# Optimization experiments

Measured on AMD Instinct MI355X. Metric: run time of the kernel, lower is better.

## Reference

```python
import jax, jax.numpy as jnp
import numpy as np

DIM = 1024
NUM_HEADS = 16
HEAD_DIM = DIM // NUM_HEADS
SCALE = HEAD_DIM ** -0.5


def setup_inputs() -> dict:
    key = jax.random.key(0)
    ks = jax.random.split(key, 9)
    s = 1.0 / np.sqrt(DIM)
    x = jax.random.normal(ks[0], (2, 2048, DIM), dtype=jnp.float32)
    Wq = jax.random.normal(ks[1], (DIM, DIM), dtype=jnp.float32) * s
    Wk = jax.random.normal(ks[2], (DIM, DIM), dtype=jnp.float32) * s
    Wv = jax.random.normal(ks[3], (DIM, DIM), dtype=jnp.float32) * s
    Wp = jax.random.normal(ks[4], (DIM, DIM), dtype=jnp.float32) * s
    bq = jax.random.normal(ks[5], (DIM,), dtype=jnp.float32) * s
    bk = jax.random.normal(ks[6], (DIM,), dtype=jnp.float32) * s
    bv = jax.random.normal(ks[7], (DIM,), dtype=jnp.float32) * s
    bp = jax.random.normal(ks[8], (DIM,), dtype=jnp.float32) * s
    return {"x": x, "Wq": Wq, "bq": bq, "Wk": Wk, "bk": bk,
            "Wv": Wv, "bv": bv, "Wp": Wp, "bp": bp}


def reference(x, Wq, bq, Wk, bk, Wv, bv, Wp, bp):
    B, L, C = x.shape
    H, D = NUM_HEADS, HEAD_DIM
    # Linear projections (torch Linear: x @ W.T + b)
    q = x @ Wq.T + bq
    k = x @ Wk.T + bk
    v = x @ Wv.T + bv
    # (B, L, H*D) -> (B, H, L, D)
    q = q.reshape(B, L, H, D).transpose(0, 2, 1, 3)
    k = k.reshape(B, L, H, D).transpose(0, 2, 1, 3)
    v = v.reshape(B, L, H, D).transpose(0, 2, 1, 3)
    # scaled dot-product attention, full L x L scores (as in source)
    attn = jnp.einsum('bhqd,bhkd->bhqk', q, k) * SCALE
    attn = jax.nn.softmax(attn, axis=-1)
    out = jnp.einsum('bhqk,bhkd->bhqd', attn, v)
    out = out.transpose(0, 2, 1, 3).reshape(B, L, C)
    return out @ Wp.T + bp
```

## Files before the change

### kernel.cpp

```cpp
#include <hip/hip_runtime.h>

#define DIMC 1024
#define SEQL 2048
#define NB   2
#define NH   16
#define HD   64
#define MTOT (NB*SEQL)
#define XSTR 2048
static constexpr float SM_SCALE = 0.125f;
static constexpr float LOG2E    = 1.4426950408889634f;
static constexpr float QSCALE   = SM_SCALE * LOG2E;

typedef short s16x8 __attribute__((ext_vector_type(8)));
typedef short s16x4 __attribute__((ext_vector_type(4)));
typedef float f32x4 __attribute__((ext_vector_type(4)));
typedef int   i32x4 __attribute__((ext_vector_type(4)));

__device__ __forceinline__ unsigned short f2bf(float f) {
    unsigned int u = __float_as_uint(f);
    u += 0x7fffu + ((u >> 16) & 1u);
    return (unsigned short)(u >> 16);
}
__device__ __forceinline__ s16x8 ld8(const unsigned short* p) {
    return *(const s16x8*)p;
}
__device__ __forceinline__ void gld_lds16(const unsigned short* g, unsigned short* l) {
    __builtin_amdgcn_global_load_lds(
        (const __attribute__((address_space(1))) void*)g,
        (__attribute__((address_space(3))) void*)l, 16, 0, 0);
}
__device__ __forceinline__ unsigned int cvtpk(float lo, float hi) {
    unsigned int r;
    asm("v_cvt_pk_bf16_f32 %0, %1, %2" : "=v"(r) : "v"(lo), "v"(hi));
    return r;
}

#define BAR()     asm volatile("s_barrier" ::: "memory")
#define WAITVM8() asm volatile("s_waitcnt vmcnt(8)" ::: "memory")
#define WAITVM4() asm volatile("s_waitcnt vmcnt(4)" ::: "memory")
#define WAITVM0() asm volatile("s_waitcnt vmcnt(0)" ::: "memory")

__global__ __launch_bounds__(256) void cast_all(
    const float* __restrict__ x,
    const float* __restrict__ Wq, const float* __restrict__ Wk,
    const float* __restrict__ Wv, const float* __restrict__ Wp,
    const float* __restrict__ bq, const float* __restrict__ bk,
    const float* __restrict__ bvv,
    unsigned short* __restrict__ xb, unsigned short* __restrict__ wall,
    float* __restrict__ ball)
{
    const int bid = blockIdx.x, tid = threadIdx.x;
    if (bid < 4096) {
        int i = bid * 256 + tid;
        float4 f = ((const float4*)x)[i];
        s16x4 o;
        o[0] = (short)f2bf(f.x); o[1] = (short)f2bf(f.y);
        o[2] = (short)f2bf(f.z); o[3] = (short)f2bf(f.w);
        ((s16x4*)xb)[i] = o;
    } else if (bid < 8192) {
        int j = (bid - 4096) * 256 + tid;
        int r = j >> 18;
        const float* src = (r == 0) ? Wq : (r == 1) ? Wk : (r == 2) ? Wv : Wp;
        float4 f = ((const float4*)src)[j & 262143];
        s16x4 o;
        o[0] = (short)f2bf(f.x); o[1] = (short)f2bf(f.y);
        o[2] = (short)f2bf(f.z); o[3] = (short)f2bf(f.w);
        ((s16x4*)wall)[j] = o;
    } else {
        int t2 = (bid - 8192) * 256 + tid;
        if (t2 < 3072)
            ball[t2] = (t2 < 1024) ? bq[t2]
                     : (t2 < 2048) ? bk[t2 - 1024] : bvv[t2 - 2048];
    }
}

__global__ __launch_bounds__(256) void gemm_tile(
    const unsigned short* __restrict__ A, int astride,
    const unsigned short* __restrict__ Wb,
    const float* __restrict__ bias,
    unsigned short* qk, unsigned short* vtb, float* outf, int mode)
{
    __shared__ __align__(16) unsigned short Asm[3][128 * 32];
    __shared__ __align__(16) unsigned short Bsm[3][128 * 32];

    const int t    = threadIdx.x;
    const int lane = t & 63;
    const int l15  = lane & 15;
    const int quad = lane >> 4;
    const int w    = t >> 6;
    const int mrow = (w & 1) * 64;
    const int ncol = (w >> 1) * 64;
    const int nt_total = (int)gridDim.x >> 5;
    const int xcd = blockIdx.x & 7;
    const int i2  = blockIdx.x >> 3;
    const int nt  = xcd * (nt_total >> 3) + (i2 >> 5);
    const int mt  = i2 & 31;
    const int row0 = mt * 128;

    const unsigned short* ga = A  + (size_t)(row0 + (t >> 2)) * astride + (t & 3) * 8;
    const unsigned short* gb = Wb + (size_t)(nt * 128 + (t >> 2)) * DIMC + (t & 3) * 8;
    const size_t gaStep = (size_t)64 * astride;
    const size_t gbStep = (size_t)64 * DIMC;

    f32x4 acc[4][4] = {};

    auto stage = [&](unsigned short* Ab, unsigned short* Bb, int k0) {
        gld_lds16(ga + k0,          Ab + t * 8);
        gld_lds16(ga + gaStep + k0, Ab + 2048 + t * 8);
        gld_lds16(gb + k0,          Bb + t * 8);
        gld_lds16(gb + gbStep + k0, Bb + 2048 + t * 8);
    };

    auto compute = [&](const unsigned short* Ac, const unsigned short* Bc) {
        s16x8 a[4], b[4];
#pragma unroll
        for (int mi = 0; mi < 4; ++mi)
            a[mi] = *(const s16x8*)(Ac + (mrow + mi * 16 + l15) * 32 + quad * 8);
#pragma unroll
        for (int ni = 0; ni < 4; ++ni)
            b[ni] = *(const s16x8*)(Bc + (ncol + ni * 16 + l15) * 32 + quad * 8);
        __builtin_amdgcn_s_setprio(1);
#pragma unroll
        for (int mi = 0; mi < 4; ++mi)
#pragma unroll
            for (int ni = 0; ni < 4; ++ni)
                acc[mi][ni] = __builtin_amdgcn_mfma_f32_16x16x32_bf16(
                    a[mi], b[ni], acc[mi][ni], 0, 0, 0);
        __builtin_amdgcn_s_setprio(0);
    };

    stage(Asm[0], Bsm[0], 0);
    stage(Asm[1], Bsm[1], 32);

#pragma unroll 1
    for (int k0 = 0; k0 < 960; k0 += 96) {
        stage(Asm[2], Bsm[2], k0 + 64);
        WAITVM8();
        BAR();
        compute(Asm[0], Bsm[0]);
        BAR();
        stage(Asm[0], Bsm[0], k0 + 96);
        WAITVM8();
        BAR();
        compute(Asm[1], Bsm[1]);
        BAR();
        stage(Asm[1], Bsm[1], k0 + 128);
        WAITVM8();
        BAR();
        compute(Asm[2], Bsm[2]);
        BAR();
    }
    WAITVM4();
    BAR();
    compute(Asm[0], Bsm[0]);
    BAR();
    WAITVM0();
    BAR();
    compute(Asm[1], Bsm[1]);

    const int proj = nt >> 3;
#pragma unroll
    for (int ni = 0; ni < 4; ++ni) {
        const int cq = (nt & 7) * 128 + ncol + ni * 16 + l15;
        const float bz = bias[proj * 1024 + cq];
#pragma unroll
        for (int mi = 0; mi < 4; ++mi) {
            const int rbase = row0 + mrow + mi * 16 + quad * 4;
            if (mode == 0) {
                if (proj < 2) {
                    const float scale = (proj == 0) ? QSCALE : 1.0f;
#pragma unroll
                    for (int r = 0; r < 4; ++r)
                        qk[(size_t)(rbase + r) * XSTR + proj * DIMC + cq] =
                            f2bf((acc[mi][ni][r] + bz) * scale);
                } else {
                    const int h = cq >> 6, d = cq & 63;
                    const int bb = rbase >> 11, ll = rbase & (SEQL - 1);
                    s16x4 v4;
                    v4[0] = (short)f2bf(acc[mi][ni][0] + bz);
                    v4[1] = (short)f2bf(acc[mi][ni][1] + bz);
                    v4[2] = (short)f2bf(acc[mi][ni][2] + bz);
                    v4[3] = (short)f2bf(acc[mi][ni][3] + bz);
                    *(s16x4*)(vtb + ((size_t)((bb * NH + h) * HD + d)) * SEQL + ll) = v4;
                }
            } else {
#pragma unroll
                for (int r = 0; r < 4; ++r)
                    outf[(size_t)(rbase + r) * DIMC + cq] = acc[mi][ni][r] + bz;
            }
        }
    }
}

__global__ __launch_bounds__(256) void attn_fused(
    unsigned short* xqk,
    const unsigned short* __restrict__ vt)
{
    __shared__ __align__(16) unsigned short Ksm[2][64 * 64];
    __shared__ __align__(16) unsigned short Vsm[2][64 * 64];

    const int t    = threadIdx.x;
    const int lane = t & 63;
    const int l15  = lane & 15;
    const int quad = lane >> 4;
    const int w    = t >> 6;

    const int xcd = blockIdx.x & 7;
    const int ii  = blockIdx.x >> 3;
    const int bh  = (xcd << 2) | (ii >> 4);
    const int qb  = ii & 15;
    const int h  = bh & (NH - 1);
    const int bb = bh >> 4;
    const int q0A = qb * 128 + w * 16;
    const int q0B = q0A + 64;

    unsigned short* qbase = xqk + (size_t)(bb * SEQL) * XSTR + h * HD + quad * 8;
    unsigned short* qrA = qbase + (size_t)(q0A + l15) * XSTR;
    unsigned short* qrB = qbase + (size_t)(q0B + l15) * XSTR;
    const s16x8 bqA0 = ld8(qrA), bqA1 = ld8(qrA + 32);
    const s16x8 bqB0 = ld8(qrB), bqB1 = ld8(qrB + 32);

    s16x8 bones;
#pragma unroll
    for (int e = 0; e < 8; ++e) bones[e] = (short)0x3F80;

    const int tr = t >> 3, tp = t & 7;
    const int swz = (tp ^ (tr & 7)) * 8;
    const unsigned short* kg = xqk + (size_t)bb * SEQL * XSTR + DIMC + h * HD
                               + (size_t)tr * XSTR + swz;
    const unsigned short* vg = vt + (size_t)(bh * HD + tr) * SEQL + swz;

    f32x4 oA[4] = {}, oB[4] = {};
    f32x4 laccA = {}, laccB = {};
    const int xk = l15 & 7;

    auto stage = [&](unsigned short* Kb, unsigned short* Vb, int j) {
#pragma unroll
        for (int g = 0; g < 2; ++g) {
            gld_lds16(kg + (size_t)(j + g * 32) * XSTR, Kb + g * 2048 + t * 8);
            gld_lds16(vg + (size_t)(g * 32) * SEQL + j,  Vb + g * 2048 + t * 8);
        }
    };

    auto compute = [&](const unsigned short* Kc, const unsigned short* Vc) {
#pragma unroll
        for (int hf = 0; hf < 2; ++hf) {
            const int k0 = (hf * 32 + l15) * 64;
            const int k1 = (hf * 32 + 16 + l15) * 64;
            s16x8 a00 = *(const s16x8*)(Kc + k0 + ((quad       ^ xk) * 8));
            s16x8 a01 = *(const s16x8*)(Kc + k0 + (((quad + 4) ^ xk) * 8));
            s16x8 a10 = *(const s16x8*)(Kc + k1 + ((quad       ^ xk) * 8));
            s16x8 a11 = *(const s16x8*)(Kc + k1 + (((quad + 4) ^ xk) * 8));

            s16x8 bv[4];
#pragma unroll
            for (int c = 0; c < 4; ++c) {
                const unsigned short* va = Vc + (c * 16 + l15) * 64 + (quad & 1) * 4;
                const int kc0 = hf * 4 + (quad >> 1);
                s16x4 v0 = *(const s16x4*)(va + ((kc0       ^ xk) * 8));
                s16x4 v1 = *(const s16x4*)(va + (((kc0 + 2) ^ xk) * 8));
                bv[c] = __builtin_shufflevector(v0, v1, 0, 1, 2, 3, 4, 5, 6, 7);
            }

            __builtin_amdgcn_s_setprio(1);
            {
                f32x4 st0 = {}, st1 = {};
                st0 = __builtin_amdgcn_mfma_f32_16x16x32_bf16(a00, bqA0, st0, 0, 0, 0);
                st0 = __builtin_amdgcn_mfma_f32_16x16x32_bf16(a01, bqA1, st0, 0, 0, 0);
                st1 = __builtin_amdgcn_mfma_f32_16x16x32_bf16(a10, bqA0, st1, 0, 0, 0);
                st1 = __builtin_amdgcn_mfma_f32_16x16x32_bf16(a11, bqA1, st1, 0, 0, 0);
                i32x4 api;
                api[0] = (int)cvtpk(__builtin_amdgcn_exp2f(st0[0]),
                                    __builtin_amdgcn_exp2f(st0[1]));
                api[1] = (int)cvtpk(__builtin_amdgcn_exp2f(st0[2]),
                                    __builtin_amdgcn_exp2f(st0[3]));
                api[2] = (int)cvtpk(__builtin_amdgcn_exp2f(st1[0]),
                                    __builtin_amdgcn_exp2f(st1[1]));
                api[3] = (int)cvtpk(__builtin_amdgcn_exp2f(st1[2]),
                                    __builtin_amdgcn_exp2f(st1[3]));
                s16x8 ap = __builtin_bit_cast(s16x8, api);
                laccA = __builtin_amdgcn_mfma_f32_16x16x32_bf16(ap, bones, laccA, 0, 0, 0);
#pragma unroll
                for (int c = 0; c < 4; ++c)
                    oA[c] = __builtin_amdgcn_mfma_f32_16x16x32_bf16(ap, bv[c], oA[c], 0, 0, 0);
            }
            {
                f32x4 st0 = {}, st1 = {};
                st0 = __builtin_amdgcn_mfma_f32_16x16x32_bf16(a00, bqB0, st0, 0, 0, 0);
                st0 = __builtin_amdgcn_mfma_f32_16x16x32_bf16(a01, bqB1, st0, 0, 0, 0);
                st1 = __builtin_amdgcn_mfma_f32_16x16x32_bf16(a10, bqB0, st1, 0, 0, 0);
                st1 = __builtin_amdgcn_mfma_f32_16x16x32_bf16(a11, bqB1, st1, 0, 0, 0);
                i32x4 api;
                api[0] = (int)cvtpk(__builtin_amdgcn_exp2f(st0[0]),
                                    __builtin_amdgcn_exp2f(st0[1]));
                api[1] = (int)cvtpk(__builtin_amdgcn_exp2f(st0[2]),
                                    __builtin_amdgcn_exp2f(st0[3]));
                api[2] = (int)cvtpk(__builtin_amdgcn_exp2f(st1[0]),
                                    __builtin_amdgcn_exp2f(st1[1]));
                api[3] = (int)cvtpk(__builtin_amdgcn_exp2f(st1[2]),
                                    __builtin_amdgcn_exp2f(st1[3]));
                s16x8 ap = __builtin_bit_cast(s16x8, api);
                laccB = __builtin_amdgcn_mfma_f32_16x16x32_bf16(ap, bones, laccB, 0, 0, 0);
#pragma unroll
                for (int c = 0; c < 4; ++c)
                    oB[c] = __builtin_amdgcn_mfma_f32_16x16x32_bf16(ap, bv[c], oB[c], 0, 0, 0);
            }
            __builtin_amdgcn_s_setprio(0);
        }
    };

    stage(Ksm[0], Vsm[0], 0);

#pragma unroll 1
    for (int jt = 0; jt < SEQL / 64; jt += 2) {
        const int j0 = jt * 64;
        stage(Ksm[1], Vsm[1], j0 + 64);
        WAITVM4();
        BAR();
        compute(Ksm[0], Vsm[0]);
        BAR();
        if (jt + 2 < SEQL / 64) {
            stage(Ksm[0], Vsm[0], j0 + 128);
            WAITVM4();
        } else {
            WAITVM0();
        }
        BAR();
        compute(Ksm[1], Vsm[1]);
        BAR();
    }

    float liA[4], liB[4];
#pragma unroll
    for (int r = 0; r < 4; ++r) {
        liA[r] = 1.0f / laccA[r];
        liB[r] = 1.0f / laccB[r];
    }

#pragma unroll
    for (int c = 0; c < 4; ++c) {
        const int d = c * 16 + l15;
#pragma unroll
        for (int r = 0; r < 4; ++r) {
            const int qr = quad * 4 + r;
            xqk[(size_t)(bb * SEQL + q0A + qr) * XSTR + h * HD + d] = f2bf(oA[c][r] * liA[r]);
            xqk[(size_t)(bb * SEQL + q0B + qr) * XSTR + h * HD + d] = f2bf(oB[c][r] * liB[r]);
        }
    }
}

extern "C" void kernel_launch(void* const* d_in, const int* in_sizes, int n_in,
                              void* d_out, int out_size, void* d_ws, size_t ws_size,
                              hipStream_t stream) {
    const float* x  = (const float*)d_in[0];
    const float* Wq = (const float*)d_in[1];
    const float* bq = (const float*)d_in[2];
    const float* Wk = (const float*)d_in[3];
    const float* bk = (const float*)d_in[4];
    const float* Wv = (const float*)d_in[5];
    const float* bv = (const float*)d_in[6];
    const float* Wp = (const float*)d_in[7];
    const float* bp = (const float*)d_in[8];
    float* out = (float*)d_out;
    unsigned short* vtb = (unsigned short*)d_out;
    unsigned short* xqk = (unsigned short*)d_in[0];

    unsigned short* ws   = (unsigned short*)d_ws;
    const size_t XELT = (size_t)MTOT * DIMC;
    const size_t WELT = (size_t)DIMC * DIMC;
    unsigned short* xb   = ws;
    unsigned short* wall = ws + XELT;
    float*          ball = (float*)(ws + 2 * XELT);

    cast_all<<<8204, 256, 0, stream>>>(x, Wq, Wk, Wv, Wp, bq, bk, bv, xb, wall, ball);

    gemm_tile<<<768, 256, 0, stream>>>(xb, DIMC, wall, ball, xqk, vtb, nullptr, 0);

    attn_fused<<<NB * NH * (SEQL / 128), 256, 0, stream>>>(xqk, vtb);

    gemm_tile<<<256, 256, 0, stream>>>(xqk, XSTR, wall + 3 * WELT, bp,
                                       nullptr, nullptr, out, 1);
}
```

Before: 212.4 us.

## Replace QKV projection GEMM with 256x256-tile 8-wave pipelined kernel

Adds a dedicated QKV projection kernel that uses 256x256 output tiles, 512 threads (8 waves), and 128KB of dynamic LDS. It double-buffers 64-wide K slices with direct global-to-LDS loads interleaved between MFMA phases, and raises wave priority around the MFMA bursts. The larger tiles raise arithmetic intensity and reduce the grid from 768 to 192 blocks. The trade-off is fewer blocks than CUs on MI355X, so some CUs idle, and higher register pressure from the 8x4 accumulator array per wave.

Measured after the change: 200.3 us. -5.7%, faster.

```diff
diff --git a/kernel.cpp b/kernel.cpp
--- a/kernel.cpp
+++ b/kernel.cpp
@@ -74,6 +74,129 @@
     }
 }
 
+__global__ __launch_bounds__(512, 2) void qkv8(
+    const unsigned short* __restrict__ A,
+    const unsigned short* __restrict__ Wb,
+    const float* __restrict__ bias,
+    unsigned short* __restrict__ qk, unsigned short* __restrict__ vtb)
+{
+    extern __shared__ __align__(16) unsigned short lds[];
+    unsigned short* lA = lds;
+    unsigned short* lB = lds + 32768;
+
+    const int t    = threadIdx.x;
+    const int lane = t & 63;
+    const int l15  = lane & 15;
+    const int quad = lane >> 4;
+    const int w    = t >> 6;
+    const int wm   = w >> 2;
+    const int wn   = w & 3;
+
+    const int xcd = blockIdx.x & 7;
+    const int lb  = xcd * 24 + (blockIdx.x >> 3);
+    const int nt  = lb >> 4;
+    const int mt  = lb & 15;
+    const int row0 = mt * 256;
+
+    const int scol = (((t & 3) ^ ((t >> 3) & 3)) * 8);
+    const unsigned short* gaQ = A  + (size_t)(row0 + (t >> 2)) * 1024 + scol;
+    const unsigned short* gbQ = Wb + (size_t)(nt * 256 + (t >> 2)) * 1024 + scol;
+
+    const int xq = (quad ^ ((l15 >> 1) & 3)) * 8;
+
+    f32x4 acc[8][4] = {};
+
+    auto stA = [&](int b, int ks, int kt2) {
+        const unsigned short* s = gaQ + (size_t)kt2 * 64 + ks * 32;
+        unsigned short* d = lA + (size_t)(b * 2 + ks) * 8192 + t * 8;
+        gld_lds16(s, d);
+        gld_lds16(s + (size_t)128 * 1024, d + 4096);
+    };
+    auto stB = [&](int b, int ks, int kt2) {
+        const unsigned short* s = gbQ + (size_t)kt2 * 64 + ks * 32;
+        unsigned short* d = lB + (size_t)(b * 2 + ks) * 8192 + t * 8;
+        gld_lds16(s, d);
+        gld_lds16(s + (size_t)128 * 1024, d + 4096);
+    };
+
+    auto doPhase = [&](const unsigned short* Ak, const unsigned short* Bk,
+                       int mh, auto&& iss, int vm) {
+        s16x8 fa[4], fb[4];
+#pragma unroll
+        for (int m = 0; m < 4; ++m)
+            fa[m] = *(const s16x8*)(Ak + (wm * 128 + mh * 64 + m * 16 + l15) * 32 + xq);
+#pragma unroll
+        for (int n = 0; n < 4; ++n)
+            fb[n] = *(const s16x8*)(Bk + (wn * 64 + n * 16 + l15) * 32 + xq);
+        iss();
+        if (vm == 8)      WAITVM8();
+        else if (vm == 4) WAITVM4();
+        else if (vm == 0) WAITVM0();
+        BAR();
+        __builtin_amdgcn_s_setprio(1);
+#pragma unroll
+        for (int m = 0; m < 4; ++m)
+#pragma unroll
+            for (int n = 0; n < 4; ++n)
+                acc[mh * 4 + m][n] = __builtin_amdgcn_mfma_f32_16x16x32_bf16(
+                    fa[m], fb[n], acc[mh * 4 + m][n], 0, 0, 0);
+        __builtin_amdgcn_s_setprio(0);
+        BAR();
+    };
+
+    auto tile = [&](int b, int kt, int mode) {
+        const unsigned short* Ak0 = lA + (size_t)b * 16384;
+        const unsigned short* Bk0 = lB + (size_t)b * 16384;
+        doPhase(Ak0, Bk0, 0, [&] { if (mode < 2) stA(b ^ 1, 1, kt + 1); }, -1);
+        doPhase(Ak0, Bk0, 1, [&] { if (mode < 2) stB(b ^ 1, 1, kt + 1); },
+                mode == 2 ? 0 : 8);
+        doPhase(Ak0 + 8192, Bk0 + 8192, 0, [&] { if (mode == 0) stA(b, 0, kt + 2); }, -1);
+        doPhase(Ak0 + 8192, Bk0 + 8192, 1, [&] { if (mode == 0) stB(b, 0, kt + 2); },
+                mode == 0 ? 8 : (mode == 1 ? 4 : -1));
+    };
+
+    stA(0, 0, 0); stB(0, 0, 0);
+    stA(0, 1, 0); stB(0, 1, 0);
+    stA(1, 0, 1); stB(1, 0, 1);
+    WAITVM4();
+    BAR();
+
+#pragma unroll 1
+    for (int kt = 0; kt < 14; kt += 2) {
+        tile(0, kt, 0);
+        tile(1, kt + 1, 0);
+    }
+    tile(0, 14, 1);
+    tile(1, 15, 2);
+
+    const int proj = nt >> 2;
+#pragma unroll
+    for (int ni = 0; ni < 4; ++ni) {
+        const int cq = (nt & 3) * 256 + wn * 64 + ni * 16 + l15;
+        const float bz = bias[proj * 1024 + cq];
+#pragma unroll
+        for (int mi = 0; mi < 8; ++mi) {
+            const int rbase = row0 + wm * 128 + mi * 16 + quad * 4;
+            if (proj < 2) {
+                const float scale = (proj == 0) ? QSCALE : 1.0f;
+#pragma unroll
+                for (int r = 0; r < 4; ++r)
+                    qk[(size_t)(rbase + r) * XSTR + proj * DIMC + cq] =
+                        f2bf((acc[mi][ni][r] + bz) * scale);
+            } else {
+                const int h = cq >> 6, d = cq & 63;
+                const int bb2 = rbase >> 11, ll = rbase & (SEQL - 1);
+                s16x4 v4;
+                v4[0] = (short)f2bf(acc[mi][ni][0] + bz);
+                v4[1] = (short)f2bf(acc[mi][ni][1] + bz);
+                v4[2] = (short)f2bf(acc[mi][ni][2] + bz);
+                v4[3] = (short)f2bf(acc[mi][ni][3] + bz);
+                *(s16x4*)(vtb + ((size_t)((bb2 * NH + h) * HD + d)) * SEQL + ll) = v4;
+            }
+        }
+    }
+}
+
 __global__ __launch_bounds__(256) void gemm_tile(
     const unsigned short* __restrict__ A, int astride,
     const unsigned short* __restrict__ Wb,
@@ -372,9 +495,17 @@
     unsigned short* wall = ws + XELT;
     float*          ball = (float*)(ws + 2 * XELT);
 
+    static bool ldsInit = false;
+    if (!ldsInit) {
+        (void)hipFuncSetAttribute((const void*)qkv8,
+                                  hipFuncAttributeMaxDynamicSharedMemorySize,
+                                  131072);
+        ldsInit = true;
+    }
+
     cast_all<<<8204, 256, 0, stream>>>(x, Wq, Wk, Wv, Wp, bq, bk, bv, xb, wall, ball);
 
-    gemm_tile<<<768, 256, 0, stream>>>(xb, DIMC, wall, ball, xqk, vtb, nullptr, 0);
+    qkv8<<<192, 512, 131072, stream>>>(xb, wall, ball, xqk, vtb);
 
     attn_fused<<<NB * NH * (SEQL / 128), 256, 0, stream>>>(xqk, vtb);
 
```
